# Optimization experiments

Hardware: AMD Instinct MI355X
Metric: run time of the kernel (lower is better)

## Reference

```python
import jax, jax.numpy as jnp
import numpy as np

TEMP = 8.0      # config.router_temp
TOP_K = 2       # config.moe_top_k
EPS = 1e-8
LN_EPS = 1e-5


def _layer_norm_noaffine(x):
    # nn.LayerNorm(input_dim, elementwise_affine=False)
    mu = jnp.mean(x, axis=-1, keepdims=True)
    var = jnp.var(x, axis=-1, keepdims=True)
    return (x - mu) / jnp.sqrt(var + LN_EPS)


def _unit_norm(x):
    # x / x.norm(dim=-1).clamp(min=EPS)
    n = jnp.linalg.norm(x, axis=-1, keepdims=True)
    return x / jnp.maximum(n, EPS)


def setup_inputs() -> dict:
    key = jax.random.key(0)
    k1, k2 = jax.random.split(key)
    x = jax.random.normal(k1, (4, 4096, 2048), dtype=jnp.float32)
    prototypes = jax.random.normal(k2, (64, 2048), dtype=jnp.float32)
    return {"x": x, "prototypes": prototypes}


def reference(x, prototypes):
    # input_norm_fn = 'norm_d', proto_norm_fn = 'unit'
    xn = _layer_norm_noaffine(x)          # [b, s, d]
    pn = _unit_norm(prototypes)           # [e, d]
    logits = jnp.einsum('bsd,ed->bse', xn, pn) / TEMP   # [b, s, e]
    probs = jax.nn.softmax(logits, axis=-1)
    top_w, top_i = jax.lax.top_k(probs, TOP_K)          # [b, s, k]
    top_w = top_w / jnp.sum(top_w, axis=-1, keepdims=True)
    return top_w, top_i
```

## Files before the change

### kernel.cpp

```cpp
#include <hip/hip_runtime.h>
#include <math.h>

typedef __attribute__((ext_vector_type(8))) short short8;
typedef __attribute__((ext_vector_type(4))) float f32x4;

constexpr int kD   = 2048;
constexpr int kE   = 64;
constexpr int kM   = 32;
constexpr int kBK  = 128;
constexpr int kIt  = kD / kBK;
constexpr int kLds = 136;

__global__ __launch_bounds__(256) void proto_prep(const float* __restrict__ p,
                                                  float* __restrict__ ws) {
  const int e   = blockIdx.x;
  const int tid = threadIdx.x;
  const float4* row = (const float4*)(p + (size_t)e * kD);
  float s = 0.f, q = 0.f;
  for (int j = tid; j < kD / 4; j += 256) {
    float4 v = row[j];
    s += (v.x + v.y) + (v.z + v.w);
    q = fmaf(v.x, v.x, fmaf(v.y, v.y, fmaf(v.z, v.z, fmaf(v.w, v.w, q))));
  }
  #pragma unroll
  for (int off = 32; off >= 1; off >>= 1) {
    s += __shfl_xor(s, off, 64);
    q += __shfl_xor(q, off, 64);
  }
  __shared__ float as[4], aq[4];
  if ((tid & 63) == 0) { as[tid >> 6] = s; aq[tid >> 6] = q; }
  __syncthreads();
  if (tid == 0) {
    float S = (as[0] + as[1]) + (as[2] + as[3]);
    float Q = (aq[0] + aq[1]) + (aq[2] + aq[3]);
    ws[e]      = S;
    ws[kE + e] = 1.f / fmaxf(sqrtf(Q), 1e-8f);
  }
}

__device__ __forceinline__ void split3(float v, unsigned& h, unsigned& m, unsigned& l) {
  unsigned u = __float_as_uint(v);
  h = u & 0xFFFF0000u;
  float r1 = v - __uint_as_float(h);
  m = __float_as_uint(r1) & 0xFFFF0000u;
  float r2 = r1 - __uint_as_float(m);
  l = __float_as_uint(r2);
}

__device__ __forceinline__ void pack2(float e0, float e1,
                                      unsigned& dh, unsigned& dm, unsigned& dl) {
  unsigned h0, m0, l0, h1, m1, l1;
  split3(e0, h0, m0, l0);
  split3(e1, h1, m1, l1);
  dh = (h0 >> 16) | h1;
  dm = (m0 >> 16) | m1;
  dl = (l0 >> 16) | (l1 & 0xFFFF0000u);
}

union FragU { short8 s; unsigned u[4]; };

__global__ __launch_bounds__(256, 2) void router_main(
    const float* __restrict__ x, const float* __restrict__ p,
    const float* __restrict__ ws, float* __restrict__ out_w,
    float* __restrict__ out_i) {
  __shared__ unsigned short sXh[kM * kLds];
  __shared__ unsigned short sXm[kM * kLds];
  __shared__ unsigned short sXl[kM * kLds];
  __shared__ float sLogit[kM * 68];
  __shared__ float sStats[kM][2];

  const int t    = threadIdx.x;
  const int w    = t >> 6;
  const int lane = t & 63;
  const int ln15 = lane & 15;
  const int q    = lane >> 4;
  const int tok0 = blockIdx.x * kM;

  const float* xg = x + (size_t)tok0 * kD;
  const int pe = w * 16 + ln15;

  f32x4 acc[2];
  acc[0] = (f32x4){0.f, 0.f, 0.f, 0.f};
  acc[1] = (f32x4){0.f, 0.f, 0.f, 0.f};
  float sx[4] = {0.f, 0.f, 0.f, 0.f}, sxx[4] = {0.f, 0.f, 0.f, 0.f};

  float4 pf[4];
  #pragma unroll
  for (int j = 0; j < 4; ++j) {
    int f = t + 256 * j;
    pf[j] = *(const float4*)(xg + (size_t)(f >> 5) * kD + (f & 31) * 4);
  }

  for (int it = 0; it < kIt; ++it) {
    __syncthreads();
    #pragma unroll
    for (int j = 0; j < 4; ++j) {
      int f   = t + 256 * j;
      int row = f >> 5, c4 = f & 31;
      float4 v = pf[j];
      sx[j] += (v.x + v.y) + (v.z + v.w);
      sxx[j] = fmaf(v.x, v.x, fmaf(v.y, v.y, fmaf(v.z, v.z, fmaf(v.w, v.w, sxx[j]))));
      unsigned dh0, dm0, dl0, dh1, dm1, dl1;
      pack2(v.x, v.y, dh0, dm0, dl0);
      pack2(v.z, v.w, dh1, dm1, dl1);
      int off = row * kLds + c4 * 4;
      *(uint2*)&sXh[off] = make_uint2(dh0, dh1);
      *(uint2*)&sXm[off] = make_uint2(dm0, dm1);
      *(uint2*)&sXl[off] = make_uint2(dl0, dl1);
    }
    __syncthreads();
    if (it + 1 < kIt) {
      #pragma unroll
      for (int j = 0; j < 4; ++j) {
        int f = t + 256 * j;
        pf[j] = *(const float4*)(xg + (size_t)(f >> 5) * kD + (it + 1) * kBK + (f & 31) * 4);
      }
    }
    #pragma unroll
    for (int c = 0; c < 4; ++c) {
      const float* pb = p + (size_t)pe * kD + it * kBK + c * 32 + q * 8;
      float4 b0 = *(const float4*)(pb);
      float4 b1 = *(const float4*)(pb + 4);
      FragU bh, bm, bl;
      pack2(b0.x, b0.y, bh.u[0], bm.u[0], bl.u[0]);
      pack2(b0.z, b0.w, bh.u[1], bm.u[1], bl.u[1]);
      pack2(b1.x, b1.y, bh.u[2], bm.u[2], bl.u[2]);
      pack2(b1.z, b1.w, bh.u[3], bm.u[3], bl.u[3]);
      #pragma unroll
      for (int m = 0; m < 2; ++m) {
        int ro = (m * 16 + ln15) * kLds + c * 32 + q * 8;
        short8 ah = *(const short8*)&sXh[ro];
        short8 am = *(const short8*)&sXm[ro];
        short8 al = *(const short8*)&sXl[ro];
        acc[m] = __builtin_amdgcn_mfma_f32_16x16x32_bf16(ah, bh.s, acc[m], 0, 0, 0);
        acc[m] = __builtin_amdgcn_mfma_f32_16x16x32_bf16(ah, bm.s, acc[m], 0, 0, 0);
        acc[m] = __builtin_amdgcn_mfma_f32_16x16x32_bf16(am, bh.s, acc[m], 0, 0, 0);
        acc[m] = __builtin_amdgcn_mfma_f32_16x16x32_bf16(am, bm.s, acc[m], 0, 0, 0);
        acc[m] = __builtin_amdgcn_mfma_f32_16x16x32_bf16(ah, bl.s, acc[m], 0, 0, 0);
        acc[m] = __builtin_amdgcn_mfma_f32_16x16x32_bf16(al, bh.s, acc[m], 0, 0, 0);
      }
    }
  }

  #pragma unroll
  for (int j = 0; j < 4; ++j) {
    float a = sx[j], b = sxx[j];
    #pragma unroll
    for (int off = 16; off >= 1; off >>= 1) {
      a += __shfl_xor(a, off, 64);
      b += __shfl_xor(b, off, 64);
    }
    if ((lane & 31) == 0) {
      int row = (t >> 5) + 8 * j;
      sStats[row][0] = a;
      sStats[row][1] = b;
    }
  }

  #pragma unroll
  for (int m = 0; m < 2; ++m)
    #pragma unroll
    for (int i = 0; i < 4; ++i) {
      int tok = m * 16 + q * 4 + i;
      sLogit[tok * 68 + w * 16 + ln15] = acc[m][i];
    }
  __syncthreads();

  const float Se  = ws[lane];
  const float inv = ws[kE + lane];
  #pragma unroll
  for (int tl = 0; tl < 8; ++tl) {
    int tk = w * 8 + tl;
    float Sx = sStats[tk][0], Sq = sStats[tk][1];
    float mu   = Sx * (1.f / kD);
    float var  = Sq * (1.f / kD) - mu * mu;
    float rstd = rsqrtf(var + 1e-5f);
    float logit = (sLogit[tk * 68 + lane] - mu * Se) * rstd * inv * 0.125f;

    float v1 = logit; int i1 = lane;
    #pragma unroll
    for (int off = 32; off >= 1; off >>= 1) {
      float ov = __shfl_xor(v1, off, 64);
      int   oi = __shfl_xor(i1, off, 64);
      if (ov > v1 || (ov == v1 && oi < i1)) { v1 = ov; i1 = oi; }
    }
    float ml = (lane == i1) ? -3.402823466e38f : logit;
    float v2 = ml; int i2 = lane;
    #pragma unroll
    for (int off = 32; off >= 1; off >>= 1) {
      float ov = __shfl_xor(v2, off, 64);
      int   oi = __shfl_xor(i2, off, 64);
      if (ov > v2 || (ov == v2 && oi < i2)) { v2 = ov; i2 = oi; }
    }
    if (lane == 0) {
      int tg = tok0 + tk;
      float er = expf(v2 - v1);
      float r  = 1.f / (1.f + er);
      out_w[2 * tg]     = r;
      out_w[2 * tg + 1] = er * r;
      out_i[2 * tg]     = (float)i1;
      out_i[2 * tg + 1] = (float)i2;
    }
  }
}

extern "C" void kernel_launch(void* const* d_in, const int* in_sizes, int n_in,
                              void* d_out, int out_size, void* d_ws, size_t ws_size,
                              hipStream_t stream) {
  const float* x = (const float*)d_in[0];
  const float* p = (const float*)d_in[1];
  float* ws = (float*)d_ws;
  const int T = in_sizes[0] / kD;
  float* out_w = (float*)d_out;
  float* out_i = (float*)d_out + (size_t)T * 2;

  proto_prep<<<kE, 256, 0, stream>>>(p, ws);
  router_main<<<T / kM, 256, 0, stream>>>(x, p, ws, out_w, out_i);
}
```

Before: 225.5 us.

## Pre-split prototypes into bf16x3 fragment layout once; halve token tile

The prototype prep kernel now splits each prototype into hi/mid/lo bf16 planes and stores them in a global buffer already arranged in MFMA fragment order. The main kernel then loads B fragments straight from that buffer instead of re-splitting fp32 prototypes in every block. The token tile shrinks from 32 to 16 so each wave does one MFMA row block, and occupancy is raised to 4 blocks per CU. The LDS A layout is also changed to interleave the three planes per fragment. In exchange, prototype fragments are re-read from global memory once per 16 tokens instead of once per 32.

```diff
diff --git a/kernel.cpp b/kernel.cpp
--- a/kernel.cpp
+++ b/kernel.cpp
@@ -4,39 +4,15 @@
 typedef __attribute__((ext_vector_type(8))) short short8;
 typedef __attribute__((ext_vector_type(4))) float f32x4;
 
-constexpr int kD   = 2048;
-constexpr int kE   = 64;
-constexpr int kM   = 32;
-constexpr int kBK  = 128;
-constexpr int kIt  = kD / kBK;
-constexpr int kLds = 136;
-
-__global__ __launch_bounds__(256) void proto_prep(const float* __restrict__ p,
-                                                  float* __restrict__ ws) {
-  const int e   = blockIdx.x;
-  const int tid = threadIdx.x;
-  const float4* row = (const float4*)(p + (size_t)e * kD);
-  float s = 0.f, q = 0.f;
-  for (int j = tid; j < kD / 4; j += 256) {
-    float4 v = row[j];
-    s += (v.x + v.y) + (v.z + v.w);
-    q = fmaf(v.x, v.x, fmaf(v.y, v.y, fmaf(v.z, v.z, fmaf(v.w, v.w, q))));
-  }
-  #pragma unroll
-  for (int off = 32; off >= 1; off >>= 1) {
-    s += __shfl_xor(s, off, 64);
-    q += __shfl_xor(q, off, 64);
-  }
-  __shared__ float as[4], aq[4];
-  if ((tid & 63) == 0) { as[tid >> 6] = s; aq[tid >> 6] = q; }
-  __syncthreads();
-  if (tid == 0) {
-    float S = (as[0] + as[1]) + (as[2] + as[3]);
-    float Q = (aq[0] + aq[1]) + (aq[2] + aq[3]);
-    ws[e]      = S;
-    ws[kE + e] = 1.f / fmaxf(sqrtf(Q), 1e-8f);
-  }
-}
+constexpr int kD  = 2048;
+constexpr int kE  = 64;
+constexpr int kM  = 16;
+constexpr int kBK = 128;
+constexpr int kIt = kD / kBK;
+constexpr int kCS = 3136;
+
+constexpr int kPlaneU = 4 * 64 * 512;
+__device__ unsigned short g_B[3 * kPlaneU];
 
 __device__ __forceinline__ void split3(float v, unsigned& h, unsigned& m, unsigned& l) {
   unsigned u = __float_as_uint(v);
@@ -57,142 +33,160 @@
   dl = (l0 >> 16) | (l1 & 0xFFFF0000u);
 }
 
-union FragU { short8 s; unsigned u[4]; };
-
-__global__ __launch_bounds__(256, 2) void router_main(
-    const float* __restrict__ x, const float* __restrict__ p,
-    const float* __restrict__ ws, float* __restrict__ out_w,
-    float* __restrict__ out_i) {
-  __shared__ unsigned short sXh[kM * kLds];
-  __shared__ unsigned short sXm[kM * kLds];
-  __shared__ unsigned short sXl[kM * kLds];
+__global__ __launch_bounds__(256) void proto_prep(const float* __restrict__ p,
+                                                  float* __restrict__ ws) {
+  const int e = blockIdx.x, t = threadIdx.x;
+  const float* row = p + (size_t)e * kD;
+  float4 v0 = *(const float4*)(row + 8 * t);
+  float4 v1 = *(const float4*)(row + 8 * t + 4);
+
+  unsigned dh[4], dm[4], dl[4];
+  pack2(v0.x, v0.y, dh[0], dm[0], dl[0]);
+  pack2(v0.z, v0.w, dh[1], dm[1], dl[1]);
+  pack2(v1.x, v1.y, dh[2], dm[2], dl[2]);
+  pack2(v1.z, v1.w, dh[3], dm[3], dl[3]);
+  const int gc = t >> 2, o = t & 3;
+  size_t base = (size_t)((e >> 4) * 64 + gc) * 512 + (16 * o + (e & 15)) * 8;
+  *(uint4*)&g_B[base]               = make_uint4(dh[0], dh[1], dh[2], dh[3]);
+  *(uint4*)&g_B[kPlaneU + base]     = make_uint4(dm[0], dm[1], dm[2], dm[3]);
+  *(uint4*)&g_B[2 * kPlaneU + base] = make_uint4(dl[0], dl[1], dl[2], dl[3]);
+
+  float s = (v0.x + v0.y) + (v0.z + v0.w) + (v1.x + v1.y) + (v1.z + v1.w);
+  float q = v0.x*v0.x + v0.y*v0.y + v0.z*v0.z + v0.w*v0.w
+          + v1.x*v1.x + v1.y*v1.y + v1.z*v1.z + v1.w*v1.w;
+  #pragma unroll
+  for (int off = 32; off >= 1; off >>= 1) {
+    s += __shfl_xor(s, off, 64);
+    q += __shfl_xor(q, off, 64);
+  }
+  __shared__ float as[4], aq[4];
+  if ((t & 63) == 0) { as[t >> 6] = s; aq[t >> 6] = q; }
+  __syncthreads();
+  if (t == 0) {
+    float S = (as[0] + as[1]) + (as[2] + as[3]);
+    float Q = (aq[0] + aq[1]) + (aq[2] + aq[3]);
+    ws[e]      = S;
+    ws[kE + e] = 1.f / fmaxf(sqrtf(Q), 1e-8f);
+  }
+}
+
+__global__ __launch_bounds__(256, 4) void router_main(
+    const float* __restrict__ x, const float* __restrict__ ws,
+    float* __restrict__ out_w, float* __restrict__ out_i) {
+  __shared__ __align__(16) unsigned char sA[4 * kCS];
   __shared__ float sLogit[kM * 68];
   __shared__ float sStats[kM][2];
 
   const int t    = threadIdx.x;
   const int w    = t >> 6;
-  const int lane = t & 63;
-  const int ln15 = lane & 15;
-  const int q    = lane >> 4;
+  const int L    = t & 63;
+  const int ln15 = L & 15;
+  const int q    = L >> 4;
   const int tok0 = blockIdx.x * kM;
-
   const float* xg = x + (size_t)tok0 * kD;
-  const int pe = w * 16 + ln15;
-
-  f32x4 acc[2];
-  acc[0] = (f32x4){0.f, 0.f, 0.f, 0.f};
-  acc[1] = (f32x4){0.f, 0.f, 0.f, 0.f};
-  float sx[4] = {0.f, 0.f, 0.f, 0.f}, sxx[4] = {0.f, 0.f, 0.f, 0.f};
-
-  float4 pf[4];
-  #pragma unroll
-  for (int j = 0; j < 4; ++j) {
-    int f = t + 256 * j;
-    pf[j] = *(const float4*)(xg + (size_t)(f >> 5) * kD + (f & 31) * 4);
+
+  f32x4 acc = (f32x4){0.f, 0.f, 0.f, 0.f};
+  float sx[2] = {0.f, 0.f}, sxx[2] = {0.f, 0.f};
+
+  float4 pf[2];
+  #pragma unroll
+  for (int jj = 0; jj < 2; ++jj) {
+    int f = t + 256 * jj;
+    pf[jj] = *(const float4*)(xg + (size_t)(f >> 5) * kD + (f & 31) * 4);
   }
 
   for (int it = 0; it < kIt; ++it) {
     __syncthreads();
     #pragma unroll
-    for (int j = 0; j < 4; ++j) {
-      int f   = t + 256 * j;
-      int row = f >> 5, c4 = f & 31;
-      float4 v = pf[j];
-      sx[j] += (v.x + v.y) + (v.z + v.w);
-      sxx[j] = fmaf(v.x, v.x, fmaf(v.y, v.y, fmaf(v.z, v.z, fmaf(v.w, v.w, sxx[j]))));
+    for (int jj = 0; jj < 2; ++jj) {
+      int f = t + 256 * jj;
+      int c4 = f & 31, k = 4 * c4;
+      int m = f >> 5, c = k >> 5, o = (k >> 3) & 3, j = k & 7;
+      float4 v = pf[jj];
+      sx[jj] += (v.x + v.y) + (v.z + v.w);
+      sxx[jj] = fmaf(v.x, v.x, fmaf(v.y, v.y, fmaf(v.z, v.z, fmaf(v.w, v.w, sxx[jj]))));
       unsigned dh0, dm0, dl0, dh1, dm1, dl1;
       pack2(v.x, v.y, dh0, dm0, dl0);
       pack2(v.z, v.w, dh1, dm1, dl1);
-      int off = row * kLds + c4 * 4;
-      *(uint2*)&sXh[off] = make_uint2(dh0, dh1);
-      *(uint2*)&sXm[off] = make_uint2(dm0, dm1);
-      *(uint2*)&sXl[off] = make_uint2(dl0, dl1);
+      unsigned char* dst = sA + c * kCS + (16 * o + m) * 48 + o * 16 + j * 2;
+      *(uint2*)(dst)      = make_uint2(dh0, dh1);
+      *(uint2*)(dst + 16) = make_uint2(dm0, dm1);
+      *(uint2*)(dst + 32) = make_uint2(dl0, dl1);
     }
     __syncthreads();
     if (it + 1 < kIt) {
       #pragma unroll
-      for (int j = 0; j < 4; ++j) {
-        int f = t + 256 * j;
-        pf[j] = *(const float4*)(xg + (size_t)(f >> 5) * kD + (it + 1) * kBK + (f & 31) * 4);
+      for (int jj = 0; jj < 2; ++jj) {
+        int f = t + 256 * jj;
+        pf[jj] = *(const float4*)(xg + (size_t)(f >> 5) * kD + (it + 1) * kBK + (f & 31) * 4);
       }
     }
     #pragma unroll
     for (int c = 0; c < 4; ++c) {
-      const float* pb = p + (size_t)pe * kD + it * kBK + c * 32 + q * 8;
-      float4 b0 = *(const float4*)(pb);
-      float4 b1 = *(const float4*)(pb + 4);
-      FragU bh, bm, bl;
-      pack2(b0.x, b0.y, bh.u[0], bm.u[0], bl.u[0]);
-      pack2(b0.z, b0.w, bh.u[1], bm.u[1], bl.u[1]);
-      pack2(b1.x, b1.y, bh.u[2], bm.u[2], bl.u[2]);
-      pack2(b1.z, b1.w, bh.u[3], bm.u[3], bl.u[3]);
-      #pragma unroll
-      for (int m = 0; m < 2; ++m) {
-        int ro = (m * 16 + ln15) * kLds + c * 32 + q * 8;
-        short8 ah = *(const short8*)&sXh[ro];
-        short8 am = *(const short8*)&sXm[ro];
-        short8 al = *(const short8*)&sXl[ro];
-        acc[m] = __builtin_amdgcn_mfma_f32_16x16x32_bf16(ah, bh.s, acc[m], 0, 0, 0);
-        acc[m] = __builtin_amdgcn_mfma_f32_16x16x32_bf16(ah, bm.s, acc[m], 0, 0, 0);
-        acc[m] = __builtin_amdgcn_mfma_f32_16x16x32_bf16(am, bh.s, acc[m], 0, 0, 0);
-        acc[m] = __builtin_amdgcn_mfma_f32_16x16x32_bf16(am, bm.s, acc[m], 0, 0, 0);
-        acc[m] = __builtin_amdgcn_mfma_f32_16x16x32_bf16(ah, bl.s, acc[m], 0, 0, 0);
-        acc[m] = __builtin_amdgcn_mfma_f32_16x16x32_bf16(al, bh.s, acc[m], 0, 0, 0);
-      }
-    }
-  }
-
-  #pragma unroll
-  for (int j = 0; j < 4; ++j) {
-    float a = sx[j], b = sxx[j];
+      const int gc = it * 4 + c;
+      const size_t bo = (size_t)(w * 64 + gc) * 512 + L * 8;
+      short8 bh = *(const short8*)&g_B[bo];
+      short8 bm = *(const short8*)&g_B[kPlaneU + bo];
+      short8 bl = *(const short8*)&g_B[2 * kPlaneU + bo];
+      const unsigned char* ra = sA + c * kCS + L * 48 + (L >> 4) * 16;
+      short8 ah = *(const short8*)(ra);
+      short8 am = *(const short8*)(ra + 16);
+      short8 al = *(const short8*)(ra + 32);
+      acc = __builtin_amdgcn_mfma_f32_16x16x32_bf16(ah, bh, acc, 0, 0, 0);
+      acc = __builtin_amdgcn_mfma_f32_16x16x32_bf16(ah, bm, acc, 0, 0, 0);
+      acc = __builtin_amdgcn_mfma_f32_16x16x32_bf16(am, bh, acc, 0, 0, 0);
+      acc = __builtin_amdgcn_mfma_f32_16x16x32_bf16(am, bm, acc, 0, 0, 0);
+      acc = __builtin_amdgcn_mfma_f32_16x16x32_bf16(ah, bl, acc, 0, 0, 0);
+      acc = __builtin_amdgcn_mfma_f32_16x16x32_bf16(al, bh, acc, 0, 0, 0);
+    }
+  }
+
+  #pragma unroll
+  for (int jj = 0; jj < 2; ++jj) {
+    float a = sx[jj], b = sxx[jj];
     #pragma unroll
     for (int off = 16; off >= 1; off >>= 1) {
       a += __shfl_xor(a, off, 64);
       b += __shfl_xor(b, off, 64);
     }
-    if ((lane & 31) == 0) {
-      int row = (t >> 5) + 8 * j;
-      sStats[row][0] = a;
-      sStats[row][1] = b;
-    }
-  }
-
-  #pragma unroll
-  for (int m = 0; m < 2; ++m)
-    #pragma unroll
-    for (int i = 0; i < 4; ++i) {
-      int tok = m * 16 + q * 4 + i;
-      sLogit[tok * 68 + w * 16 + ln15] = acc[m][i];
-    }
+    if ((L & 31) == 0) {
+      int m = (t >> 5) + 8 * jj;
+      sStats[m][0] = a;
+      sStats[m][1] = b;
+    }
+  }
+
+  #pragma unroll
+  for (int i = 0; i < 4; ++i)
+    sLogit[(q * 4 + i) * 68 + w * 16 + ln15] = acc[i];
   __syncthreads();
 
-  const float Se  = ws[lane];
-  const float inv = ws[kE + lane];
-  #pragma unroll
-  for (int tl = 0; tl < 8; ++tl) {
-    int tk = w * 8 + tl;
-    float Sx = sStats[tk][0], Sq = sStats[tk][1];
-    float mu   = Sx * (1.f / kD);
-    float var  = Sq * (1.f / kD) - mu * mu;
+  const float Se  = ws[L];
+  const float inv = ws[kE + L];
+  #pragma unroll
+  for (int tl = 0; tl < 4; ++tl) {
+    int tk = w * 4 + tl;
+    float mu   = sStats[tk][0] * (1.f / kD);
+    float var  = sStats[tk][1] * (1.f / kD) - mu * mu;
     float rstd = rsqrtf(var + 1e-5f);
-    float logit = (sLogit[tk * 68 + lane] - mu * Se) * rstd * inv * 0.125f;
-
-    float v1 = logit; int i1 = lane;
+    float logit = (sLogit[tk * 68 + L] - mu * Se) * rstd * inv * 0.125f;
+
+    float v1 = logit; int i1 = L;
     #pragma unroll
     for (int off = 32; off >= 1; off >>= 1) {
       float ov = __shfl_xor(v1, off, 64);
       int   oi = __shfl_xor(i1, off, 64);
       if (ov > v1 || (ov == v1 && oi < i1)) { v1 = ov; i1 = oi; }
     }
-    float ml = (lane == i1) ? -3.402823466e38f : logit;
-    float v2 = ml; int i2 = lane;
+    float ml = (L == i1) ? -3.402823466e38f : logit;
+    float v2 = ml; int i2 = L;
     #pragma unroll
     for (int off = 32; off >= 1; off >>= 1) {
       float ov = __shfl_xor(v2, off, 64);
       int   oi = __shfl_xor(i2, off, 64);
       if (ov > v2 || (ov == v2 && oi < i2)) { v2 = ov; i2 = oi; }
     }
-    if (lane == 0) {
+    if (L == 0) {
       int tg = tok0 + tk;
       float er = expf(v2 - v1);
       float r  = 1.f / (1.f + er);
@@ -215,5 +209,5 @@
   float* out_i = (float*)d_out + (size_t)T * 2;
 
   proto_prep<<<kE, 256, 0, stream>>>(p, ws);
-  router_main<<<T / kM, 256, 0, stream>>>(x, p, ws, out_w, out_i);
-}
+  router_main<<<T / kM, 256, 0, stream>>>(x, ws, out_w, out_i);
+}
```

New measurement: 225.2 us. About the same (-0.1%).
